# Kernel tuning notes

Hardware: AMD Instinct MI355X
Metric: run time of the kernel (lower is better)

## Reference

```python
import jax, jax.numpy as jnp
import numpy as np

N_NODES = 100000
N_EDGES = 3200000
NCLASSES = 4
IN_DIM = 2          # per-node feature dim -> edge in_feats = 2*IN_DIM = 4
HID = 8             # output_dim


def setup_inputs() -> dict:
    key = jax.random.key(0)
    k_m, k_e, k_w1, k_b1, k_w2, k_b2 = jax.random.split(key, 6)
    m = jax.random.normal(k_m, (N_NODES, NCLASSES, IN_DIM), dtype=jnp.float32)
    edge_index = jax.random.randint(k_e, (2, N_EDGES), 0, N_NODES, dtype=jnp.int64)
    in_feats = 2 * IN_DIM
    # ClasswiseLinear: one independent Linear per class (grouped weights)
    s1 = 1.0 / np.sqrt(in_feats)
    s2 = 1.0 / np.sqrt(HID)
    W1 = jax.random.uniform(k_w1, (NCLASSES, in_feats, HID), jnp.float32, -s1, s1)
    b1 = jax.random.uniform(k_b1, (NCLASSES, HID), jnp.float32, -s1, s1)
    W2 = jax.random.uniform(k_w2, (NCLASSES, HID, 1), jnp.float32, -s2, s2)
    b2 = jax.random.uniform(k_b2, (NCLASSES, 1), jnp.float32, -s2, s2)
    return {"m": m, "edge_index": edge_index, "W1": W1, "b1": b1, "W2": W2, "b2": b2}


def reference(m, edge_index, W1, b1, W2, b2):
    row, col = edge_index[0], edge_index[1]
    # gather node features per edge; concat dest/src -> [E, C, 2*IN_DIM]
    B = jnp.concatenate([m[col], m[row]], axis=-1)
    B = jax.lax.stop_gradient(B)  # original code calls .detach()
    # classwise linear 1 + tanh: grouped GEMM over class axis c
    h = jnp.tanh(jnp.einsum("eci,cih->ech", B, W1) + b1)      # [E, C, HID]
    o = jnp.tanh(jnp.einsum("ech,cho->eco", h, W2) + b2)      # [E, C, 1]
    # softmax over the class dimension (dim=1)
    return jax.nn.softmax(o, axis=1)
```

## Files before the change

kernel.cpp:

```cpp
#include <hip/hip_runtime.h>

#define TWO_LOG2E 2.8853901817779268f
#define LOG2E     1.4426950408889634f

typedef float f32x2 __attribute__((ext_vector_type(2)));

template<int CTRL>
__device__ __forceinline__ float dpp_qperm(float x) {
    int r = __builtin_amdgcn_update_dpp(0, __float_as_int(x), CTRL, 0xF, 0xF, true);
    return __int_as_float(r);
}

__device__ __forceinline__ f32x2 splat2(float s) { f32x2 v; v.x = s; v.y = s; return v; }

__global__ __launch_bounds__(256) void edge_mlp(
    const float* __restrict__ m,
    const int*   __restrict__ eidx,
    const float* __restrict__ W1,
    const float* __restrict__ b1,
    const float* __restrict__ W2,
    const float* __restrict__ b2,
    float*       __restrict__ out,
    const int nE)
{
    __shared__ __align__(16) float sw1[4 * 36];
    __shared__ __align__(16) float sbw[4 * 18];
    __shared__ float so0[4];

    const int tidb = threadIdx.x;
    if (tidb < 128) {
        const int c = tidb >> 5, r = tidb & 31, i = r >> 3, j = r & 7;
        sw1[c * 36 + (j >> 1) * 8 + i * 2 + (j & 1)] =
            W1[c * 32 + i * 8 + j] * TWO_LOG2E;
    } else if (tidb < 192) {
        const int q = tidb - 128, c = q >> 4, r = q & 15, p = r >> 2, k = r & 3;
        const int j = 2 * p + (k & 1);
        sbw[c * 18 + p * 4 + k] =
            (k < 2) ? b1[c * 8 + j] * TWO_LOG2E
                    : W2[c * 8 + j] * (-2.0f * TWO_LOG2E);
    } else if (tidb < 196) {
        const int c = tidb - 192;
        float s = b2[c];
        #pragma unroll
        for (int j = 0; j < 8; ++j) s += W2[c * 8 + j];
        so0[c] = s * TWO_LOG2E;
    }
    __syncthreads();

    const int tid0 = blockIdx.x * blockDim.x + threadIdx.x;
    const int c = tid0 & 3;
    const int cc2 = c * 2;
    const float* w1c = sw1 + c * 36;
    const f32x2* bwc = (const f32x2*)(sbw + c * 18);
    const float o0 = so0[c];

    const int* eidx1 = eidx + nE;
    const int total  = nE * 4;
    const int stride = gridDim.x * blockDim.x;

    constexpr int UN = 4;
    int t = tid0;

    for (; t + (UN - 1) * stride < total; t += UN * stride) {
        int row[UN], col[UN];
        #pragma unroll
        for (int k = 0; k < UN; ++k) {
            const int e = (t + k * stride) >> 2;
            row[k] = __builtin_nontemporal_load(eidx  + e);
            col[k] = __builtin_nontemporal_load(eidx1 + e);
        }
        f32x2 mc[UN], mr[UN];
        #pragma unroll
        for (int k = 0; k < UN; ++k) {
            mc[k] = *(const f32x2*)(m + (unsigned)col[k] * 8u + cc2);
            mr[k] = *(const f32x2*)(m + (unsigned)row[k] * 8u + cc2);
        }
        #pragma unroll
        for (int k = 0; k < UN; ++k) {
            float o = o0;
            #pragma unroll
            for (int p = 0; p < 4; ++p) {
                const f32x2* wp = (const f32x2*)(w1c + p * 8);
                f32x2 h = bwc[p * 2];
                h = __builtin_elementwise_fma(splat2(mc[k].x), wp[0], h);
                h = __builtin_elementwise_fma(splat2(mc[k].y), wp[1], h);
                h = __builtin_elementwise_fma(splat2(mr[k].x), wp[2], h);
                h = __builtin_elementwise_fma(splat2(mr[k].y), wp[3], h);
                const float a0 = __builtin_amdgcn_exp2f(h.x) + 1.0f;
                const float a1 = __builtin_amdgcn_exp2f(h.y) + 1.0f;
                const float inv = __builtin_amdgcn_rcpf(a0 * a1);
                const f32x2 w2n01 = bwc[p * 2 + 1];
                o = fmaf(w2n01.x, inv * a1, o);
                o = fmaf(w2n01.y, inv * a0, o);
            }
            const float e2 = __builtin_amdgcn_exp2f(o);
            const float r2 = __builtin_amdgcn_rcpf(e2 + 1.0f);
            const float eo = __builtin_amdgcn_exp2f(fmaf(-TWO_LOG2E, r2, LOG2E));
            float s = eo + dpp_qperm<0xB1>(eo);
            s = s + dpp_qperm<0x4E>(s);
            __builtin_nontemporal_store(eo * __builtin_amdgcn_rcpf(s),
                                        out + (t + k * stride));
        }
    }

    for (; t < total; t += stride) {
        const int e  = t >> 2;
        const int r0 = eidx[e];
        const int c0 = eidx1[e];
        const f32x2 mcv = *(const f32x2*)(m + (unsigned)c0 * 8u + cc2);
        const f32x2 mrv = *(const f32x2*)(m + (unsigned)r0 * 8u + cc2);
        float o = o0;
        #pragma unroll
        for (int p = 0; p < 4; ++p) {
            const f32x2* wp = (const f32x2*)(w1c + p * 8);
            f32x2 h = bwc[p * 2];
            h = __builtin_elementwise_fma(splat2(mcv.x), wp[0], h);
            h = __builtin_elementwise_fma(splat2(mcv.y), wp[1], h);
            h = __builtin_elementwise_fma(splat2(mrv.x), wp[2], h);
            h = __builtin_elementwise_fma(splat2(mrv.y), wp[3], h);
            const float a0 = __builtin_amdgcn_exp2f(h.x) + 1.0f;
            const float a1 = __builtin_amdgcn_exp2f(h.y) + 1.0f;
            const float inv = __builtin_amdgcn_rcpf(a0 * a1);
            const f32x2 w2n01 = bwc[p * 2 + 1];
            o = fmaf(w2n01.x, inv * a1, o);
            o = fmaf(w2n01.y, inv * a0, o);
        }
        const float e2 = __builtin_amdgcn_exp2f(o);
        const float r2 = __builtin_amdgcn_rcpf(e2 + 1.0f);
        const float eo = __builtin_amdgcn_exp2f(fmaf(-TWO_LOG2E, r2, LOG2E));
        float s = eo + dpp_qperm<0xB1>(eo);
        s = s + dpp_qperm<0x4E>(s);
        out[t] = eo * __builtin_amdgcn_rcpf(s);
    }
}

extern "C" void kernel_launch(void* const* d_in, const int* in_sizes, int n_in,
                              void* d_out, int out_size, void* d_ws, size_t ws_size,
                              hipStream_t stream) {
    const float* m  = (const float*)d_in[0];
    const int* eidx = (const int*)d_in[1];
    const float* W1 = (const float*)d_in[2];
    const float* b1 = (const float*)d_in[3];
    const float* W2 = (const float*)d_in[4];
    const float* b2 = (const float*)d_in[5];
    float* out = (float*)d_out;
    const int nE = in_sizes[1] / 2;

    const int threads = 256;
    const int blocks  = 2048;
    hipLaunchKernelGGL(edge_mlp, dim3(blocks), dim3(threads), 0, stream,
                       m, eidx, W1, b1, W2, b2, out, nE);
}
```

Before: 55.21 us.

## Process one edge per thread across all four classes with vector loads/stores

```diff
diff --git a/kernel.cpp b/kernel.cpp
--- a/kernel.cpp
+++ b/kernel.cpp
@@ -4,16 +4,11 @@
 #define LOG2E     1.4426950408889634f
 
 typedef float f32x2 __attribute__((ext_vector_type(2)));
-
-template<int CTRL>
-__device__ __forceinline__ float dpp_qperm(float x) {
-    int r = __builtin_amdgcn_update_dpp(0, __float_as_int(x), CTRL, 0xF, 0xF, true);
-    return __int_as_float(r);
-}
+typedef float f32x4 __attribute__((ext_vector_type(4)));
 
 __device__ __forceinline__ f32x2 splat2(float s) { f32x2 v; v.x = s; v.y = s; return v; }
 
-__global__ __launch_bounds__(256) void edge_mlp(
+__global__ __launch_bounds__(256, 2) void edge_mlp(
     const float* __restrict__ m,
     const int*   __restrict__ eidx,
     const float* __restrict__ W1,
@@ -47,90 +42,131 @@
     }
     __syncthreads();
 
-    const int tid0 = blockIdx.x * blockDim.x + threadIdx.x;
-    const int c = tid0 & 3;
-    const int cc2 = c * 2;
-    const float* w1c = sw1 + c * 36;
-    const f32x2* bwc = (const f32x2*)(sbw + c * 18);
-    const float o0 = so0[c];
+    float o0r[4];
+    #pragma unroll
+    for (int c = 0; c < 4; ++c) o0r[c] = so0[c];
 
+    const int tid    = blockIdx.x * blockDim.x + threadIdx.x;
+    const int stride = gridDim.x * blockDim.x;
     const int* eidx1 = eidx + nE;
-    const int total  = nE * 4;
-    const int stride = gridDim.x * blockDim.x;
+    constexpr int UN = 4;
 
-    constexpr int UN = 4;
-    int t = tid0;
-
-    for (; t + (UN - 1) * stride < total; t += UN * stride) {
-        int row[UN], col[UN];
+    int e = tid;
+    for (; e + (UN - 1) * stride < nE; e += UN * stride) {
+        int ri[UN], ci[UN];
         #pragma unroll
         for (int k = 0; k < UN; ++k) {
-            const int e = (t + k * stride) >> 2;
-            row[k] = __builtin_nontemporal_load(eidx  + e);
-            col[k] = __builtin_nontemporal_load(eidx1 + e);
+            ri[k] = __builtin_nontemporal_load(eidx  + e + k * stride);
+            ci[k] = __builtin_nontemporal_load(eidx1 + e + k * stride);
         }
-        f32x2 mc[UN], mr[UN];
+        f32x4 A[UN], B[UN], C[UN], D[UN];
         #pragma unroll
         for (int k = 0; k < UN; ++k) {
-            mc[k] = *(const f32x2*)(m + (unsigned)col[k] * 8u + cc2);
-            mr[k] = *(const f32x2*)(m + (unsigned)row[k] * 8u + cc2);
+            const unsigned co = (unsigned)ci[k] * 8u, ro = (unsigned)ri[k] * 8u;
+            A[k] = *(const f32x4*)(m + co);  B[k] = *(const f32x4*)(m + co + 4);
+            C[k] = *(const f32x4*)(m + ro);  D[k] = *(const f32x4*)(m + ro + 4);
+        }
+
+        float eo[UN][4], ss[UN];
+        #pragma unroll
+        for (int k = 0; k < UN; ++k) ss[k] = 0.0f;
+
+        #pragma unroll
+        for (int c = 0; c < 4; ++c) {
+            const float* w1c = sw1 + c * 36;
+            const f32x2* bwc = (const f32x2*)(sbw + c * 18);
+            float o[UN];
+            #pragma unroll
+            for (int k = 0; k < UN; ++k) o[k] = o0r[c];
+            #pragma unroll
+            for (int p = 0; p < 4; ++p) {
+                const f32x2* wp   = (const f32x2*)(w1c + p * 8);
+                const f32x2 bb01  = bwc[p * 2];
+                const f32x2 w2n01 = bwc[p * 2 + 1];
+                #pragma unroll
+                for (int k = 0; k < UN; ++k) {
+                    const f32x4 lo = (c < 2) ? A[k] : B[k];
+                    const f32x4 rr = (c < 2) ? C[k] : D[k];
+                    const float mx = (c & 1) ? lo.z : lo.x;
+                    const float my = (c & 1) ? lo.w : lo.y;
+                    const float rx = (c & 1) ? rr.z : rr.x;
+                    const float ry = (c & 1) ? rr.w : rr.y;
+                    f32x2 h = bb01;
+                    h = __builtin_elementwise_fma(splat2(mx), wp[0], h);
+                    h = __builtin_elementwise_fma(splat2(my), wp[1], h);
+                    h = __builtin_elementwise_fma(splat2(rx), wp[2], h);
+                    h = __builtin_elementwise_fma(splat2(ry), wp[3], h);
+                    const float a0 = __builtin_amdgcn_exp2f(h.x) + 1.0f;
+                    const float a1 = __builtin_amdgcn_exp2f(h.y) + 1.0f;
+                    const float inv = __builtin_amdgcn_rcpf(a0 * a1);
+                    o[k] = fmaf(w2n01.x, inv * a1, o[k]);
+                    o[k] = fmaf(w2n01.y, inv * a0, o[k]);
+                }
+            }
+            #pragma unroll
+            for (int k = 0; k < UN; ++k) {
+                const float e2 = __builtin_amdgcn_exp2f(o[k]);
+                const float r2 = __builtin_amdgcn_rcpf(e2 + 1.0f);
+                const float v  = __builtin_amdgcn_exp2f(fmaf(-TWO_LOG2E, r2, LOG2E));
+                eo[k][c] = v;
+                ss[k] += v;
+            }
         }
         #pragma unroll
         for (int k = 0; k < UN; ++k) {
-            float o = o0;
+            const float rs = __builtin_amdgcn_rcpf(ss[k]);
+            f32x4 res;
+            res.x = eo[k][0] * rs; res.y = eo[k][1] * rs;
+            res.z = eo[k][2] * rs; res.w = eo[k][3] * rs;
+            __builtin_nontemporal_store(res,
+                reinterpret_cast<f32x4*>(out) + (e + k * stride));
+        }
+    }
+
+    for (; e < nE; e += stride) {
+        const int r0 = eidx[e];
+        const int c0 = eidx1[e];
+        const unsigned co = (unsigned)c0 * 8u, ro = (unsigned)r0 * 8u;
+        const f32x4 A0 = *(const f32x4*)(m + co), B0 = *(const f32x4*)(m + co + 4);
+        const f32x4 C0 = *(const f32x4*)(m + ro), D0 = *(const f32x4*)(m + ro + 4);
+        float eo[4], ss = 0.0f;
+        #pragma unroll
+        for (int c = 0; c < 4; ++c) {
+            const float* w1c = sw1 + c * 36;
+            const f32x2* bwc = (const f32x2*)(sbw + c * 18);
+            const f32x4 lo = (c < 2) ? A0 : B0;
+            const f32x4 rr = (c < 2) ? C0 : D0;
+            const float mx = (c & 1) ? lo.z : lo.x;
+            const float my = (c & 1) ? lo.w : lo.y;
+            const float rx = (c & 1) ? rr.z : rr.x;
+            const float ry = (c & 1) ? rr.w : rr.y;
+            float o = o0r[c];
             #pragma unroll
             for (int p = 0; p < 4; ++p) {
-                const f32x2* wp = (const f32x2*)(w1c + p * 8);
-                f32x2 h = bwc[p * 2];
-                h = __builtin_elementwise_fma(splat2(mc[k].x), wp[0], h);
-                h = __builtin_elementwise_fma(splat2(mc[k].y), wp[1], h);
-                h = __builtin_elementwise_fma(splat2(mr[k].x), wp[2], h);
-                h = __builtin_elementwise_fma(splat2(mr[k].y), wp[3], h);
+                const f32x2* wp   = (const f32x2*)(w1c + p * 8);
+                const f32x2 bb01  = bwc[p * 2];
+                const f32x2 w2n01 = bwc[p * 2 + 1];
+                f32x2 h = bb01;
+                h = __builtin_elementwise_fma(splat2(mx), wp[0], h);
+                h = __builtin_elementwise_fma(splat2(my), wp[1], h);
+                h = __builtin_elementwise_fma(splat2(rx), wp[2], h);
+                h = __builtin_elementwise_fma(splat2(ry), wp[3], h);
                 const float a0 = __builtin_amdgcn_exp2f(h.x) + 1.0f;
                 const float a1 = __builtin_amdgcn_exp2f(h.y) + 1.0f;
                 const float inv = __builtin_amdgcn_rcpf(a0 * a1);
-                const f32x2 w2n01 = bwc[p * 2 + 1];
                 o = fmaf(w2n01.x, inv * a1, o);
                 o = fmaf(w2n01.y, inv * a0, o);
             }
             const float e2 = __builtin_amdgcn_exp2f(o);
             const float r2 = __builtin_amdgcn_rcpf(e2 + 1.0f);
-            const float eo = __builtin_amdgcn_exp2f(fmaf(-TWO_LOG2E, r2, LOG2E));
-            float s = eo + dpp_qperm<0xB1>(eo);
-            s = s + dpp_qperm<0x4E>(s);
-            __builtin_nontemporal_store(eo * __builtin_amdgcn_rcpf(s),
-                                        out + (t + k * stride));
+            eo[c] = __builtin_amdgcn_exp2f(fmaf(-TWO_LOG2E, r2, LOG2E));
+            ss += eo[c];
         }
-    }
-
-    for (; t < total; t += stride) {
-        const int e  = t >> 2;
-        const int r0 = eidx[e];
-        const int c0 = eidx1[e];
-        const f32x2 mcv = *(const f32x2*)(m + (unsigned)c0 * 8u + cc2);
-        const f32x2 mrv = *(const f32x2*)(m + (unsigned)r0 * 8u + cc2);
-        float o = o0;
-        #pragma unroll
-        for (int p = 0; p < 4; ++p) {
-            const f32x2* wp = (const f32x2*)(w1c + p * 8);
-            f32x2 h = bwc[p * 2];
-            h = __builtin_elementwise_fma(splat2(mcv.x), wp[0], h);
-            h = __builtin_elementwise_fma(splat2(mcv.y), wp[1], h);
-            h = __builtin_elementwise_fma(splat2(mrv.x), wp[2], h);
-            h = __builtin_elementwise_fma(splat2(mrv.y), wp[3], h);
-            const float a0 = __builtin_amdgcn_exp2f(h.x) + 1.0f;
-            const float a1 = __builtin_amdgcn_exp2f(h.y) + 1.0f;
-            const float inv = __builtin_amdgcn_rcpf(a0 * a1);
-            const f32x2 w2n01 = bwc[p * 2 + 1];
-            o = fmaf(w2n01.x, inv * a1, o);
-            o = fmaf(w2n01.y, inv * a0, o);
-        }
-        const float e2 = __builtin_amdgcn_exp2f(o);
-        const float r2 = __builtin_amdgcn_rcpf(e2 + 1.0f);
-        const float eo = __builtin_amdgcn_exp2f(fmaf(-TWO_LOG2E, r2, LOG2E));
-        float s = eo + dpp_qperm<0xB1>(eo);
-        s = s + dpp_qperm<0x4E>(s);
-        out[t] = eo * __builtin_amdgcn_rcpf(s);
+        const float rs = __builtin_amdgcn_rcpf(ss);
+        f32x4 res;
+        res.x = eo[0] * rs; res.y = eo[1] * rs;
+        res.z = eo[2] * rs; res.w = eo[3] * rs;
+        __builtin_nontemporal_store(res, reinterpret_cast<f32x4*>(out) + e);
     }
 }
 
@@ -147,7 +183,7 @@
     const int nE = in_sizes[1] / 2;
 
     const int threads = 256;
-    const int blocks  = 2048;
+    const int blocks  = 1536;
     hipLaunchKernelGGL(edge_mlp, dim3(blocks), dim3(threads), 0, stream,
                        m, eidx, W1, b1, W2, b2, out, nE);
 }
```

After: 85.48 us. 1.55x slower.

## Split index and node-feature loads across quad lanes and exchange via DPP

Applied to the files above, without the earlier changes.

```diff
diff --git a/kernel.cpp b/kernel.cpp
--- a/kernel.cpp
+++ b/kernel.cpp
@@ -4,16 +4,22 @@
 #define LOG2E     1.4426950408889634f
 
 typedef float f32x2 __attribute__((ext_vector_type(2)));
+typedef float f32x4 __attribute__((ext_vector_type(4)));
 
 template<int CTRL>
 __device__ __forceinline__ float dpp_qperm(float x) {
     int r = __builtin_amdgcn_update_dpp(0, __float_as_int(x), CTRL, 0xF, 0xF, true);
     return __int_as_float(r);
 }
-
+__device__ __forceinline__ f32x4 qswap4(f32x4 v) {
+    f32x4 r;
+    r.x = dpp_qperm<0xB1>(v.x); r.y = dpp_qperm<0xB1>(v.y);
+    r.z = dpp_qperm<0xB1>(v.z); r.w = dpp_qperm<0xB1>(v.w);
+    return r;
+}
 __device__ __forceinline__ f32x2 splat2(float s) { f32x2 v; v.x = s; v.y = s; return v; }
 
-__global__ __launch_bounds__(256) void edge_mlp(
+__global__ void edge_mlp(
     const float* __restrict__ m,
     const int*   __restrict__ eidx,
     const float* __restrict__ W1,
@@ -48,44 +54,47 @@
     __syncthreads();
 
     const int tid0 = blockIdx.x * blockDim.x + threadIdx.x;
-    const int c = tid0 & 3;
-    const int cc2 = c * 2;
+    const int c    = tid0 & 3;
+    const bool odd = (c & 1);
+    const unsigned halfOfs = (unsigned)((c >> 1) & 1) * 4u;
     const float* w1c = sw1 + c * 36;
     const f32x2* bwc = (const f32x2*)(sbw + c * 18);
     const float o0 = so0[c];
 
-    const int* eidx1 = eidx + nE;
-    const int total  = nE * 4;
-    const int stride = gridDim.x * blockDim.x;
+    const int* rowlist = eidx;
+    const int* collist = eidx + nE;
+    const int* mylist  = odd ? rowlist : collist;
+    const int nQuads = (gridDim.x * blockDim.x) >> 2;
 
     constexpr int UN = 4;
-    int t = tid0;
+    int e0 = tid0 >> 2;
 
-    for (; t + (UN - 1) * stride < total; t += UN * stride) {
-        int row[UN], col[UN];
+    for (; e0 + (UN - 1) * nQuads < nE; e0 += UN * nQuads) {
+        int idx[UN];
+        #pragma unroll
+        for (int k = 0; k < UN; ++k)
+            idx[k] = __builtin_nontemporal_load(mylist + e0 + k * nQuads);
+        f32x4 pc[UN];
+        #pragma unroll
+        for (int k = 0; k < UN; ++k)
+            pc[k] = *(const f32x4*)(m + (unsigned)idx[k] * 8u + halfOfs);
+
         #pragma unroll
         for (int k = 0; k < UN; ++k) {
-            const int e = (t + k * stride) >> 2;
-            row[k] = __builtin_nontemporal_load(eidx  + e);
-            col[k] = __builtin_nontemporal_load(eidx1 + e);
-        }
-        f32x2 mc[UN], mr[UN];
-        #pragma unroll
-        for (int k = 0; k < UN; ++k) {
-            mc[k] = *(const f32x2*)(m + (unsigned)col[k] * 8u + cc2);
-            mr[k] = *(const f32x2*)(m + (unsigned)row[k] * 8u + cc2);
-        }
-        #pragma unroll
-        for (int k = 0; k < UN; ++k) {
+            const f32x4 nb = qswap4(pc[k]);
+            f32x2 mc, mr;
+            mc.x = odd ? nb.z    : pc[k].x;  mc.y = odd ? nb.w    : pc[k].y;
+            mr.x = odd ? pc[k].z : nb.x;     mr.y = odd ? pc[k].w : nb.y;
+
             float o = o0;
             #pragma unroll
             for (int p = 0; p < 4; ++p) {
                 const f32x2* wp = (const f32x2*)(w1c + p * 8);
                 f32x2 h = bwc[p * 2];
-                h = __builtin_elementwise_fma(splat2(mc[k].x), wp[0], h);
-                h = __builtin_elementwise_fma(splat2(mc[k].y), wp[1], h);
-                h = __builtin_elementwise_fma(splat2(mr[k].x), wp[2], h);
-                h = __builtin_elementwise_fma(splat2(mr[k].y), wp[3], h);
+                h = __builtin_elementwise_fma(splat2(mc.x), wp[0], h);
+                h = __builtin_elementwise_fma(splat2(mc.y), wp[1], h);
+                h = __builtin_elementwise_fma(splat2(mr.x), wp[2], h);
+                h = __builtin_elementwise_fma(splat2(mr.y), wp[3], h);
                 const float a0 = __builtin_amdgcn_exp2f(h.x) + 1.0f;
                 const float a1 = __builtin_amdgcn_exp2f(h.y) + 1.0f;
                 const float inv = __builtin_amdgcn_rcpf(a0 * a1);
@@ -99,25 +108,26 @@
             float s = eo + dpp_qperm<0xB1>(eo);
             s = s + dpp_qperm<0x4E>(s);
             __builtin_nontemporal_store(eo * __builtin_amdgcn_rcpf(s),
-                                        out + (t + k * stride));
+                out + ((unsigned)(e0 + k * nQuads) << 2) + c);
         }
     }
 
-    for (; t < total; t += stride) {
-        const int e  = t >> 2;
-        const int r0 = eidx[e];
-        const int c0 = eidx1[e];
-        const f32x2 mcv = *(const f32x2*)(m + (unsigned)c0 * 8u + cc2);
-        const f32x2 mrv = *(const f32x2*)(m + (unsigned)r0 * 8u + cc2);
+    for (; e0 < nE; e0 += nQuads) {
+        const int idx = __builtin_nontemporal_load(mylist + e0);
+        const f32x4 piece = *(const f32x4*)(m + (unsigned)idx * 8u + halfOfs);
+        const f32x4 nb = qswap4(piece);
+        f32x2 mc, mr;
+        mc.x = odd ? nb.z    : piece.x;  mc.y = odd ? nb.w    : piece.y;
+        mr.x = odd ? piece.z : nb.x;     mr.y = odd ? piece.w : nb.y;
         float o = o0;
         #pragma unroll
         for (int p = 0; p < 4; ++p) {
             const f32x2* wp = (const f32x2*)(w1c + p * 8);
             f32x2 h = bwc[p * 2];
-            h = __builtin_elementwise_fma(splat2(mcv.x), wp[0], h);
-            h = __builtin_elementwise_fma(splat2(mcv.y), wp[1], h);
-            h = __builtin_elementwise_fma(splat2(mrv.x), wp[2], h);
-            h = __builtin_elementwise_fma(splat2(mrv.y), wp[3], h);
+            h = __builtin_elementwise_fma(splat2(mc.x), wp[0], h);
+            h = __builtin_elementwise_fma(splat2(mc.y), wp[1], h);
+            h = __builtin_elementwise_fma(splat2(mr.x), wp[2], h);
+            h = __builtin_elementwise_fma(splat2(mr.y), wp[3], h);
             const float a0 = __builtin_amdgcn_exp2f(h.x) + 1.0f;
             const float a1 = __builtin_amdgcn_exp2f(h.y) + 1.0f;
             const float inv = __builtin_amdgcn_rcpf(a0 * a1);
@@ -130,7 +140,7 @@
         const float eo = __builtin_amdgcn_exp2f(fmaf(-TWO_LOG2E, r2, LOG2E));
         float s = eo + dpp_qperm<0xB1>(eo);
         s = s + dpp_qperm<0x4E>(s);
-        out[t] = eo * __builtin_amdgcn_rcpf(s);
+        out[((unsigned)e0 << 2) + c] = eo * __builtin_amdgcn_rcpf(s);
     }
 }
 
```

Result: slower. 56.99 us (+3.2%).
